# Optimization experiments

Hardware: AMD Instinct MI355X
Metric: run time of the kernel (lower is better)

Reference implementation:

```python
import jax, jax.numpy as jnp
import numpy as np

N_NODES = 100000
N_EDGES = 800000
N_GRAPHS = 4000
EMB = 128      # node_emb_dims
HID = 256      # hidden_dims
FP = 2048      # fingerprint_dims
FIELD_DIMS = {"atom_type": 120, "degree": 12, "charge": 10}


def setup_inputs() -> dict:
    key = jax.random.key(0)
    ks = iter(jax.random.split(key, 40))
    p = lambda shape: jax.random.normal(next(ks), shape, dtype=jnp.float32) * 0.02
    inp = {
        "atom_idx": jax.random.randint(next(ks), (N_NODES,), 0, FIELD_DIMS["atom_type"]),
        "degree_idx": jax.random.randint(next(ks), (N_NODES,), 0, FIELD_DIMS["degree"]),
        "charge_idx": jax.random.randint(next(ks), (N_NODES,), 0, FIELD_DIMS["charge"]),
        "edge_index": jax.random.randint(next(ks), (2, N_EDGES), 0, N_NODES),
        "batch": jnp.sort(jax.random.randint(next(ks), (N_NODES,), 0, N_GRAPHS)),
        "fingerprint": jax.random.normal(next(ks), (N_GRAPHS, FP), dtype=jnp.float32),
        # FFM projector params
        "emb_atom": p((FIELD_DIMS["atom_type"], EMB)),
        "emb_degree": p((FIELD_DIMS["degree"], EMB)),
        "emb_charge": p((FIELD_DIMS["charge"], EMB)),
        "proj_w1": p((3 * EMB, EMB)), "proj_b1": jnp.zeros((EMB,), jnp.float32),
        "proj_w2": p((EMB, EMB)), "proj_b2": jnp.zeros((EMB,), jnp.float32),
        # fingerprint linear
        "fp_w": p((FP, HID)), "fp_b": jnp.zeros((HID,), jnp.float32),
        # GCN layers
        "conv_w0": p((EMB, HID)), "conv_b0": jnp.zeros((HID,), jnp.float32),
        "conv_w1": p((HID, HID)), "conv_b1": jnp.zeros((HID,), jnp.float32),
        "conv_w2": p((HID, HID)), "conv_b2": jnp.zeros((HID,), jnp.float32),
        "conv_w3": p((HID, HID)), "conv_b3": jnp.zeros((HID,), jnp.float32),
        # head
        "lin1_w": p((2 * HID, HID // 2)), "lin1_b": jnp.zeros((HID // 2,), jnp.float32),
        "lin2_w": p((HID // 2, 1)), "lin2_b": jnp.zeros((1,), jnp.float32),
    }
    return inp


def gcn_conv(x, w, b, src, dst, n):
    # PyG GCNConv: linear, add self-loops, symmetric norm, scatter-add at dst, + bias
    xw = x @ w
    loop = jnp.arange(n)
    src_f = jnp.concatenate([src, loop])
    dst_f = jnp.concatenate([dst, loop])
    deg = jax.ops.segment_sum(jnp.ones_like(dst_f, dtype=x.dtype), dst_f, num_segments=n)
    dinv = jax.lax.rsqrt(deg)  # deg >= 1 thanks to self-loops
    norm = dinv[src_f] * dinv[dst_f]                       # [E+N]
    msg = xw[src_f] * norm[:, None]                        # [E+N, HID]
    return jax.ops.segment_sum(msg, dst_f, num_segments=n) + b


def reference(atom_idx, degree_idx, charge_idx, edge_index, batch, fingerprint,
              emb_atom, emb_degree, emb_charge,
              proj_w1, proj_b1, proj_w2, proj_b2, fp_w, fp_b,
              conv_w0, conv_b0, conv_w1, conv_b1, conv_w2, conv_b2, conv_w3, conv_b3,
              lin1_w, lin1_b, lin2_w, lin2_b):
    # FieldAwareFactorizationMachine projector (vectorized over all nodes)
    e = jnp.concatenate([emb_atom[atom_idx], emb_degree[degree_idx], emb_charge[charge_idx]], axis=-1)
    h = jax.nn.relu(e @ proj_w1 + proj_b1) @ proj_w2 + proj_b2   # [N, EMB]
    src, dst = edge_index[0], edge_index[1]
    for w, b in ((conv_w0, conv_b0), (conv_w1, conv_b1), (conv_w2, conv_b2), (conv_w3, conv_b3)):
        h = jax.nn.relu(gcn_conv(h, w, b, src, dst, N_NODES))
    pooled = jax.ops.segment_sum(h, batch, num_segments=N_GRAPHS)  # scatter sum pooling
    fp_emb = fingerprint @ fp_w + fp_b
    z = jnp.concatenate([fp_emb, pooled], axis=-1)                 # [B, 2*HID]
    z = jax.nn.relu(z @ lin1_w + lin1_b)
    return z @ lin2_w + lin2_b                                     # [B, 1]
```

## Files before the change

kernel.cpp:

```cpp
#include <hip/hip_runtime.h>
#include <stdint.h>

#define NN 100000
#define NE 800000
#define NG 4000
#define NBLK ((NN + 255) / 256)

typedef __attribute__((ext_vector_type(8))) short s16x8;
typedef __attribute__((ext_vector_type(4))) float f32x4;
typedef __attribute__((ext_vector_type(2))) float f32x2;

__device__ __forceinline__ float b2f(unsigned short u) {
    return __uint_as_float(((unsigned int)u) << 16);
}
__device__ __forceinline__ unsigned short f2b(float f) {
    unsigned int x = __float_as_uint(f);
    x = x + 0x7FFFu + ((x >> 16) & 1u);
    return (unsigned short)(x >> 16);
}
__device__ __forceinline__ s16x8 cvt8(const float* __restrict__ p) {
    float4 a = *(const float4*)p;
    float4 b = *(const float4*)(p + 4);
    s16x8 r = {(short)f2b(a.x), (short)f2b(a.y), (short)f2b(a.z), (short)f2b(a.w),
               (short)f2b(b.x), (short)f2b(b.y), (short)f2b(b.z), (short)f2b(b.w)};
    return r;
}

__device__ __forceinline__ void gload16(const void* g, void* l) {
    __builtin_amdgcn_global_load_lds((const __attribute__((address_space(1))) unsigned int*)g,
                                     (__attribute__((address_space(3))) unsigned int*)l, 16, 0, 0);
}

__device__ __forceinline__ void acc8(f32x2* acc, s16x8 r) {
    const unsigned int* u = (const unsigned int*)&r;
#pragma unroll
    for (int q = 0; q < 4; ++q) {
        unsigned int w = u[q];
        f32x2 x;
        x[0] = __uint_as_float(w << 16);
        x[1] = __uint_as_float(w & 0xFFFF0000u);
        asm("v_pk_add_f32 %0, %1, %0" : "+v"(acc[q]) : "v"(x));
    }
}

__global__ void k_count(const int* __restrict__ dst, int* __restrict__ cnt) {
    int e = blockIdx.x * 256 + threadIdx.x;
    if (e < NE) atomicAdd(&cnt[dst[e]], 1);
}

__global__ void k_dinv(const int* __restrict__ cnt, float* __restrict__ dinv) {
    int n = blockIdx.x * 256 + threadIdx.x;
    if (n < NN) dinv[n] = rsqrtf((float)(cnt[n] + 1));
}

__global__ __launch_bounds__(256) void k_bsum(const int* __restrict__ cnt, int* __restrict__ bsum) {
    __shared__ int s[256];
    int i = blockIdx.x * 256 + threadIdx.x;
    s[threadIdx.x] = (i < NN) ? cnt[i] : 0;
    __syncthreads();
    for (int off = 128; off; off >>= 1) {
        if (threadIdx.x < off) s[threadIdx.x] += s[threadIdx.x + off];
        __syncthreads();
    }
    if (threadIdx.x == 0) bsum[blockIdx.x] = s[0];
}

__global__ __launch_bounds__(512) void k_bscan(const int* __restrict__ bsum, int* __restrict__ bpre) {
    __shared__ int s[512];
    int t = threadIdx.x;
    int v = (t < NBLK) ? bsum[t] : 0;
    s[t] = v;
    __syncthreads();
    for (int off = 1; off < 512; off <<= 1) {
        int u = (t >= off) ? s[t - off] : 0;
        __syncthreads();
        s[t] += u;
        __syncthreads();
    }
    if (t < NBLK) bpre[t] = s[t] - v;
}

__global__ __launch_bounds__(256) void k_rowptr(const int* __restrict__ cnt, const int* __restrict__ bpre,
                                                int* __restrict__ row_ptr, int* __restrict__ cursor) {
    __shared__ int s[256];
    int t = threadIdx.x;
    int i = blockIdx.x * 256 + t;
    int v = (i < NN) ? cnt[i] : 0;
    s[t] = v;
    __syncthreads();
    for (int off = 1; off < 256; off <<= 1) {
        int u = (t >= off) ? s[t - off] : 0;
        __syncthreads();
        s[t] += u;
        __syncthreads();
    }
    if (i < NN) {
        int excl = bpre[blockIdx.x] + s[t] - v;
        row_ptr[i] = excl;
        cursor[i] = excl;
        if (i == NN - 1) row_ptr[NN] = NE;
    }
}

__global__ void k_fill(const int* __restrict__ src, const int* __restrict__ dst,
                       int* __restrict__ cursor, int* __restrict__ colA) {
    int e = blockIdx.x * 256 + threadIdx.x;
    if (e < NE) {
        int d = dst[e];
        int p = atomicAdd(&cursor[d], 1);
        colA[p] = src[e];
    }
}

__global__ void k_t(const float* __restrict__ src, unsigned short* __restrict__ dst, int KN, int ln) {
    int i = blockIdx.x * 256 + threadIdx.x;
    if (i < KN) {
        int k = i >> ln, n = i & ((1 << ln) - 1);
        dst[(size_t)n * (KN >> ln) + k] = f2b(src[i]);
    }
}

__global__ void k_cvt(const float* __restrict__ src, unsigned short* __restrict__ dst, int n8) {
    int i = blockIdx.x * 256 + threadIdx.x;
    if (i < n8) *(s16x8*)&dst[(size_t)i * 8] = cvt8(&src[(size_t)i * 8]);
}

__global__ void k_binit(float* __restrict__ fe, const float* __restrict__ b) {
    int i = blockIdx.x * 256 + threadIdx.x;
    fe[i] = b[i & 255];
}

__global__ void k_z(const float* __restrict__ fe, unsigned short* __restrict__ zcat) {
    int i = blockIdx.x * 256 + threadIdx.x;
    int g = i >> 8, c = i & 255;
    zcat[(size_t)g * 512 + c] = f2b(fe[i]);
}

template <bool GATHER, bool BIAS, bool RELU, bool CBF16>
__global__ __launch_bounds__(256) void k_mm(
    const unsigned short* __restrict__ A, const unsigned short* __restrict__ Bt,
    void* __restrict__ Cv, const float* __restrict__ bias, int M, int N, int K,
    const int* __restrict__ ai, const int* __restrict__ di, const int* __restrict__ ci,
    const float* __restrict__ ea, const float* __restrict__ ed, const float* __restrict__ ec) {
    __shared__ unsigned short As[128 * 40];
    __shared__ unsigned short Bs[128 * 40];
    const int tid = threadIdx.x;
    const int row0 = blockIdx.x * 128, col0 = blockIdx.y * 128;
    const int lane = tid & 63, wid = tid >> 6;
    const int wrow = (wid >> 1) * 64, wcol = (wid & 1) * 64;
    const int lr = lane & 15, lk8 = (lane >> 4) * 8;

    const int sr = tid >> 1;
    const int skc = (tid & 1) * 16;
    const int agrow = row0 + sr;
    const int bgrow = col0 + sr;
    int ia = 0, idg = 0, ic = 0;
    if (GATHER && agrow < M) { ia = ai[agrow] * 128; idg = di[agrow] * 128; ic = ci[agrow] * 128; }

    f32x4 acc[4][4] = {};

    for (int kb = 0; kb < K; kb += 32) {
        if (kb) __syncthreads();
#pragma unroll
        for (int c = 0; c < 2; ++c) {
            int kloc = skc + c * 8;
            s16x8 v = {};
            if (agrow < M) {
                if (GATHER) {
                    int kg = kb + kloc;
                    const float* p = (kg < 128) ? (ea + ia + kg)
                                   : (kg < 256) ? (ed + idg + kg - 128)
                                                : (ec + ic + kg - 256);
                    v = cvt8(p);
                } else {
                    v = *(const s16x8*)&A[(size_t)agrow * K + kb + kloc];
                }
            }
            *(s16x8*)&As[sr * 40 + kloc] = v;
            s16x8 w = *(const s16x8*)&Bt[(size_t)bgrow * K + kb + kloc];
            *(s16x8*)&Bs[sr * 40 + kloc] = w;
        }
        __syncthreads();
        s16x8 af[4], bfr[4];
#pragma unroll
        for (int f = 0; f < 4; ++f)
            af[f] = *(const s16x8*)&As[(wrow + f * 16 + lr) * 40 + lk8];
#pragma unroll
        for (int f = 0; f < 4; ++f)
            bfr[f] = *(const s16x8*)&Bs[(wcol + f * 16 + lr) * 40 + lk8];
#pragma unroll
        for (int fm = 0; fm < 4; ++fm)
#pragma unroll
            for (int fn = 0; fn < 4; ++fn)
                acc[fm][fn] = __builtin_amdgcn_mfma_f32_16x16x32_bf16(af[fm], bfr[fn], acc[fm][fn], 0, 0, 0);
    }
#pragma unroll
    for (int fm = 0; fm < 4; ++fm) {
#pragma unroll
        for (int r = 0; r < 4; ++r) {
            int row = row0 + wrow + fm * 16 + (lane >> 4) * 4 + r;
            if (row < M) {
#pragma unroll
                for (int fn = 0; fn < 4; ++fn) {
                    int col = col0 + wcol + fn * 16 + lr;
                    float v = acc[fm][fn][r];
                    if (BIAS) v += bias[col];
                    if (RELU) v = fmaxf(v, 0.f);
                    if (CBF16) ((unsigned short*)Cv)[(size_t)row * N + col] = f2b(v);
                    else       ((float*)Cv)[(size_t)row * N + col] = v;
                }
            }
        }
    }
}

template <bool BIAS, bool RELU, bool CBF16, bool SPLITK, bool PRES>
__global__ __launch_bounds__(256) void k_mmA(
    const unsigned short* __restrict__ A, const unsigned short* __restrict__ Bt,
    void* __restrict__ Cv, const float* __restrict__ bias, const float* __restrict__ pres,
    int M, int N, int K, int kc) {
    __shared__ unsigned short As[128 * 32];
    __shared__ unsigned short Bs[128 * 32];
    const int tid = threadIdx.x;
    const int row0 = blockIdx.x * 128, col0 = blockIdx.y * 128;
    const int lane = tid & 63, wid = tid >> 6;
    const int wrow = (wid >> 1) * 64, wcol = (wid & 1) * 64;
    const int lr = lane & 15, lk8 = (lane >> 4) * 8;

    const int k0 = SPLITK ? blockIdx.z * kc : 0;
    const int k1 = SPLITK ? k0 + kc : K;

    const int sra = wid * 32 + (lane >> 2);
    const int sca = (lane & 3) * 8;
    const unsigned short* a0 = A + (size_t)min(row0 + sra, M - 1) * K + sca;
    const unsigned short* a1 = A + (size_t)min(row0 + sra + 16, M - 1) * K + sca;
    const unsigned short* b0 = Bt + (size_t)(col0 + sra) * K + sca;
    const unsigned short* b1 = Bt + (size_t)(col0 + sra + 16) * K + sca;
    unsigned short* lA0 = &As[(wid * 2 + 0) * 512];
    unsigned short* lA1 = &As[(wid * 2 + 1) * 512];
    unsigned short* lB0 = &Bs[(wid * 2 + 0) * 512];
    unsigned short* lB1 = &Bs[(wid * 2 + 1) * 512];

    f32x4 acc[4][4] = {};

    for (int kb = k0; kb < k1; kb += 32) {
        if (kb != k0) __syncthreads();
        gload16(a0 + kb, lA0);
        gload16(a1 + kb, lA1);
        gload16(b0 + kb, lB0);
        gload16(b1 + kb, lB1);
        __syncthreads();
        s16x8 af[4], bfr[4];
#pragma unroll
        for (int f = 0; f < 4; ++f)
            af[f] = *(const s16x8*)&As[(wrow + f * 16 + lr) * 32 + lk8];
#pragma unroll
        for (int f = 0; f < 4; ++f)
            bfr[f] = *(const s16x8*)&Bs[(wcol + f * 16 + lr) * 32 + lk8];
#pragma unroll
        for (int fm = 0; fm < 4; ++fm)
#pragma unroll
            for (int fn = 0; fn < 4; ++fn)
                acc[fm][fn] = __builtin_amdgcn_mfma_f32_16x16x32_bf16(af[fm], bfr[fn], acc[fm][fn], 0, 0, 0);
    }
#pragma unroll
    for (int fm = 0; fm < 4; ++fm) {
#pragma unroll
        for (int r = 0; r < 4; ++r) {
            int row = row0 + wrow + fm * 16 + (lane >> 4) * 4 + r;
            if (row < M) {
                float pr = PRES ? pres[row] : 1.f;
#pragma unroll
                for (int fn = 0; fn < 4; ++fn) {
                    int col = col0 + wcol + fn * 16 + lr;
                    float v = acc[fm][fn][r];
                    if (SPLITK) {
                        atomicAdd(&((float*)Cv)[(size_t)row * N + col], v);
                    } else {
                        if (BIAS) v += bias[col];
                        if (RELU) v = fmaxf(v, 0.f);
                        if (PRES) v *= pr;
                        if (CBF16) ((unsigned short*)Cv)[(size_t)row * N + col] = f2b(v);
                        else       ((float*)Cv)[(size_t)row * N + col] = v;
                    }
                }
            }
        }
    }
}

template <int WPN, bool FUSE>
__global__ __launch_bounds__(256) void k_scat2(const unsigned short* __restrict__ xw,
                                               unsigned short* __restrict__ hout,
                                               const float* __restrict__ dinv,
                                               const int* __restrict__ row_ptr,
                                               const int* __restrict__ colA,
                                               const float* __restrict__ bias) {
    constexpr int W = WPN * 128;
    const int wid = threadIdx.x >> 6, lane = threadIdx.x & 63;
    const int gw = blockIdx.x * 4 + wid;
    const int v = (WPN == 2) ? (gw >> 1) : gw;
    const int cs = (WPN == 2) ? (gw & 1) * 128 : 0;
    const int grp = lane >> 4, li = lane & 15;
    const int c0 = cs + li * 8;

    f32x2 acc[4] = {};
    const int beg = row_ptr[v], end = row_ptr[v + 1];
    int p = beg + grp;
    for (; p + 4 < end; p += 8) {
        int s0 = colA[p], s1 = colA[p + 4];
        s16x8 r0 = *(const s16x8*)&xw[(size_t)s0 * W + c0];
        s16x8 r1 = *(const s16x8*)&xw[(size_t)s1 * W + c0];
        acc8(acc, r0);
        acc8(acc, r1);
    }
    if (p < end) {
        int s0 = colA[p];
        s16x8 r0 = *(const s16x8*)&xw[(size_t)s0 * W + c0];
        acc8(acc, r0);
    }

    const float dv = dinv[v];
    s16x8 rs = *(const s16x8*)&xw[(size_t)v * W + c0];
    unsigned short o[8];
#pragma unroll
    for (int q = 0; q < 4; ++q) {
#pragma unroll
        for (int h = 0; h < 2; ++h) {
            float a = acc[q][h];
            a += __shfl_xor(a, 16);
            a += __shfl_xor(a, 32);
            a += b2f((unsigned short)rs[2 * q + h]);
            a *= dv;
            if (FUSE) a = fmaxf(a + bias[c0 + 2 * q + h], 0.f);
            o[2 * q + h] = f2b(a);
        }
    }
    if (grp == 0) *(s16x8*)&hout[(size_t)v * W + c0] = *(const s16x8*)o;
}

__global__ void k_bounds(const int* __restrict__ batch, int* __restrict__ gstart) {
    int n = blockIdx.x * 256 + threadIdx.x;
    if (n >= NN) return;
    int b = batch[n];
    if (n == 0) {
        for (int g = 0; g <= b; ++g) gstart[g] = 0;
    } else {
        int pb = batch[n - 1];
        if (pb != b)
            for (int g = pb + 1; g <= b; ++g) gstart[g] = n;
    }
    if (n == NN - 1) {
        for (int g = b + 1; g <= NG; ++g) gstart[g] = NN;
    }
}

__global__ __launch_bounds__(64) void k_pool(const unsigned short* __restrict__ h,
                                             const int* __restrict__ gstart,
                                             unsigned short* __restrict__ zcat) {
    int g = blockIdx.x;
    int lane = threadIdx.x;
    int c0 = lane * 4;
    int beg = gstart[g], end = gstart[g + 1];
    float a0 = 0.f, a1 = 0.f, a2 = 0.f, a3 = 0.f;
    for (int n = beg; n < end; ++n) {
        ushort4 r = *(const ushort4*)&h[(size_t)n * 256 + c0];
        a0 += b2f(r.x); a1 += b2f(r.y); a2 += b2f(r.z); a3 += b2f(r.w);
    }
    ushort4 o;
    o.x = f2b(a0); o.y = f2b(a1); o.z = f2b(a2); o.w = f2b(a3);
    *(ushort4*)&zcat[(size_t)g * 512 + 256 + c0] = o;
}

__global__ __launch_bounds__(256) void k_dot(const float* __restrict__ z1,
                                             const float* __restrict__ w2,
                                             const float* __restrict__ b2,
                                             float* __restrict__ out) {
    int wid = threadIdx.x >> 6, lane = threadIdx.x & 63;
    int g = blockIdx.x * 4 + wid;
    float s = z1[(size_t)g * 128 + lane] * w2[lane]
            + z1[(size_t)g * 128 + 64 + lane] * w2[64 + lane];
#pragma unroll
    for (int off = 32; off; off >>= 1) s += __shfl_xor(s, off);
    if (lane == 0) out[g] = s + b2[0];
}

extern "C" void kernel_launch(void* const* d_in, const int* in_sizes, int n_in,
                              void* d_out, int out_size, void* d_ws, size_t ws_size,
                              hipStream_t stream) {
    const int* atom_idx   = (const int*)d_in[0];
    const int* degree_idx = (const int*)d_in[1];
    const int* charge_idx = (const int*)d_in[2];
    const int* edge_index = (const int*)d_in[3];
    const int* batch      = (const int*)d_in[4];
    const float* fingerprint = (const float*)d_in[5];
    const float* emb_atom   = (const float*)d_in[6];
    const float* emb_degree = (const float*)d_in[7];
    const float* emb_charge = (const float*)d_in[8];
    const float* proj_w1 = (const float*)d_in[9];
    const float* proj_b1 = (const float*)d_in[10];
    const float* proj_w2 = (const float*)d_in[11];
    const float* proj_b2 = (const float*)d_in[12];
    const float* fp_w = (const float*)d_in[13];
    const float* fp_b = (const float*)d_in[14];
    const float* conv_w[4] = {(const float*)d_in[15], (const float*)d_in[17],
                              (const float*)d_in[19], (const float*)d_in[21]};
    const float* conv_b[4] = {(const float*)d_in[16], (const float*)d_in[18],
                              (const float*)d_in[20], (const float*)d_in[22]};
    const float* lin1_w = (const float*)d_in[23];
    const float* lin1_b = (const float*)d_in[24];
    const float* lin2_w = (const float*)d_in[25];
    const float* lin2_b = (const float*)d_in[26];
    float* out = (float*)d_out;

    const int* src = edge_index;
    const int* dst = edge_index + NE;

    char* p = (char*)d_ws;
    auto carve = [&](size_t bytes) { void* r = (void*)p; p += (bytes + 255) & ~(size_t)255; return r; };
    unsigned short* bufA = (unsigned short*)carve((size_t)NN * 256 * 2);
    unsigned short* bufB = (unsigned short*)carve((size_t)NN * 256 * 2);
    int*   cnt     = (int*)carve((size_t)NN * 4);
    float* dinv    = (float*)carve((size_t)NN * 4);
    int*   row_ptr = (int*)carve((size_t)(NN + 1) * 4);
    int*   cursor  = (int*)carve((size_t)(NN + 1) * 4);
    int*   colA    = (int*)carve((size_t)NE * 4);
    int*   gstart  = (int*)carve((size_t)(NG + 1) * 4);
    float* fp_emb  = (float*)carve((size_t)NG * 256 * 4);
    int*   bsum    = (int*)carve((size_t)NBLK * 4);
    int*   bpre    = (int*)carve((size_t)NBLK * 4);
    unsigned short* w1t  = (unsigned short*)carve((size_t)128 * 384 * 2);
    unsigned short* w2t  = (unsigned short*)carve((size_t)128 * 128 * 2);
    unsigned short* cwt[4];
    cwt[0] = (unsigned short*)carve((size_t)256 * 128 * 2);
    for (int l = 1; l < 4; ++l) cwt[l] = (unsigned short*)carve((size_t)256 * 256 * 2);
    unsigned short* fpwt = (unsigned short*)carve((size_t)256 * 2048 * 2);
    unsigned short* fpbf = (unsigned short*)carve((size_t)NG * 2048 * 2);
    unsigned short* l1wt = (unsigned short*)carve((size_t)128 * 512 * 2);
    unsigned short* zcat = (unsigned short*)carve((size_t)NG * 512 * 2);
    float* z1      = (float*)carve((size_t)NG * 128 * 4);

    hipMemsetAsync(cnt, 0, (size_t)NN * 4, stream);
    k_count<<<(NE + 255) / 256, 256, 0, stream>>>(dst, cnt);
    k_dinv<<<(NN + 255) / 256, 256, 0, stream>>>(cnt, dinv);
    k_bsum<<<NBLK, 256, 0, stream>>>(cnt, bsum);
    k_bscan<<<1, 512, 0, stream>>>(bsum, bpre);
    k_rowptr<<<NBLK, 256, 0, stream>>>(cnt, bpre, row_ptr, cursor);
    k_fill<<<(NE + 255) / 256, 256, 0, stream>>>(src, dst, cursor, colA);

    k_t<<<(49152 + 255) / 256, 256, 0, stream>>>(proj_w1, w1t, 49152, 7);
    k_t<<<(16384 + 255) / 256, 256, 0, stream>>>(proj_w2, w2t, 16384, 7);
    k_t<<<(32768 + 255) / 256, 256, 0, stream>>>(conv_w[0], cwt[0], 32768, 8);
    for (int l = 1; l < 4; ++l)
        k_t<<<(65536 + 255) / 256, 256, 0, stream>>>(conv_w[l], cwt[l], 65536, 8);
    k_t<<<(524288 + 255) / 256, 256, 0, stream>>>(fp_w, fpwt, 524288, 8);
    k_t<<<(65536 + 255) / 256, 256, 0, stream>>>(lin1_w, l1wt, 65536, 7);
    k_cvt<<<(NG * 2048 / 8 + 255) / 256, 256, 0, stream>>>(fingerprint, fpbf, NG * 2048 / 8);

    k_binit<<<NG, 256, 0, stream>>>(fp_emb, fp_b);
    k_mmA<false, false, false, true, false><<<dim3((NG + 127) / 128, 2, 4), 256, 0, stream>>>(
        fpbf, fpwt, fp_emb, nullptr, nullptr, NG, 256, 2048, 512);
    k_z<<<NG, 256, 0, stream>>>(fp_emb, zcat);

    const int mg = (NN + 127) / 128;

    k_mm<true, true, true, true><<<dim3(mg, 1), 256, 0, stream>>>(
        nullptr, w1t, bufA, proj_b1, NN, 128, 384,
        atom_idx, degree_idx, charge_idx, emb_atom, emb_degree, emb_charge);
    k_mmA<true, false, true, false, true><<<dim3(mg, 1), 256, 0, stream>>>(
        bufA, w2t, bufB, proj_b2, dinv, NN, 128, 128, 0);

    k_scat2<1, false><<<NN / 4, 256, 0, stream>>>(bufB, bufA, dinv, row_ptr, colA, nullptr);
    k_mmA<true, true, true, false, false><<<dim3(mg, 2), 256, 0, stream>>>(
        bufA, cwt[0], bufB, conv_b[0], nullptr, NN, 256, 128, 0);

    for (int l = 1; l < 4; ++l) {
        k_mmA<false, false, true, false, true><<<dim3(mg, 2), 256, 0, stream>>>(
            bufB, cwt[l], bufA, nullptr, dinv, NN, 256, 256, 0);
        k_scat2<2, true><<<NN / 2, 256, 0, stream>>>(bufA, bufB, dinv, row_ptr, colA, conv_b[l]);
    }

    k_bounds<<<(NN + 255) / 256, 256, 0, stream>>>(batch, gstart);
    k_pool<<<NG, 64, 0, stream>>>(bufB, gstart, zcat);

    k_mmA<true, true, false, false, false><<<dim3((NG + 127) / 128, 1), 256, 0, stream>>>(
        zcat, l1wt, z1, lin1_b, nullptr, NG, 128, 512, 0);
    k_dot<<<NG / 4, 256, 0, stream>>>(z1, lin2_w, lin2_b, out);
}
```

Before: 789.8 us.

## Double-buffer GEMM LDS tiles and assign one node per 16-lane group in scatter

The GEMM kernel now keeps two LDS buffers, so it can start loading the next K tile while the MFMAs run on the current one, and it needs one barrier per iteration instead of two. The scatter kernel now maps each 16-lane group (or pair of groups for width 256) to its own destination node rather than a whole wave per node, which removes the cross-group shuffle reduction and the idle lanes when degrees are small. This raises per-wave parallelism across nodes at the cost of more divergence between groups with different degrees and double the LDS use in the GEMM.

After: 749.1 us. 1.05x faster.

```diff
diff --git a/kernel.cpp b/kernel.cpp
--- a/kernel.cpp
+++ b/kernel.cpp
@@ -219,8 +219,8 @@
     const unsigned short* __restrict__ A, const unsigned short* __restrict__ Bt,
     void* __restrict__ Cv, const float* __restrict__ bias, const float* __restrict__ pres,
     int M, int N, int K, int kc) {
-    __shared__ unsigned short As[128 * 32];
-    __shared__ unsigned short Bs[128 * 32];
+    __shared__ unsigned short As[2][128 * 32];
+    __shared__ unsigned short Bs[2][128 * 32];
     const int tid = threadIdx.x;
     const int row0 = blockIdx.x * 128, col0 = blockIdx.y * 128;
     const int lane = tid & 63, wid = tid >> 6;
@@ -228,40 +228,48 @@
     const int lr = lane & 15, lk8 = (lane >> 4) * 8;
 
     const int k0 = SPLITK ? blockIdx.z * kc : 0;
-    const int k1 = SPLITK ? k0 + kc : K;
+    const int nt = (SPLITK ? kc : K) / 32;
 
     const int sra = wid * 32 + (lane >> 2);
     const int sca = (lane & 3) * 8;
-    const unsigned short* a0 = A + (size_t)min(row0 + sra, M - 1) * K + sca;
-    const unsigned short* a1 = A + (size_t)min(row0 + sra + 16, M - 1) * K + sca;
-    const unsigned short* b0 = Bt + (size_t)(col0 + sra) * K + sca;
-    const unsigned short* b1 = Bt + (size_t)(col0 + sra + 16) * K + sca;
-    unsigned short* lA0 = &As[(wid * 2 + 0) * 512];
-    unsigned short* lA1 = &As[(wid * 2 + 1) * 512];
-    unsigned short* lB0 = &Bs[(wid * 2 + 0) * 512];
-    unsigned short* lB1 = &Bs[(wid * 2 + 1) * 512];
+    const unsigned short* a0 = A + (size_t)min(row0 + sra, M - 1) * K + sca + k0;
+    const unsigned short* a1 = A + (size_t)min(row0 + sra + 16, M - 1) * K + sca + k0;
+    const unsigned short* b0 = Bt + (size_t)(col0 + sra) * K + sca + k0;
+    const unsigned short* b1 = Bt + (size_t)(col0 + sra + 16) * K + sca + k0;
+    const int lo0 = (wid * 2 + 0) * 512;
+    const int lo1 = (wid * 2 + 1) * 512;
 
     f32x4 acc[4][4] = {};
 
-    for (int kb = k0; kb < k1; kb += 32) {
-        if (kb != k0) __syncthreads();
-        gload16(a0 + kb, lA0);
-        gload16(a1 + kb, lA1);
-        gload16(b0 + kb, lB0);
-        gload16(b1 + kb, lB1);
-        __syncthreads();
+    gload16(a0, &As[0][lo0]);
+    gload16(a1, &As[0][lo1]);
+    gload16(b0, &Bs[0][lo0]);
+    gload16(b1, &Bs[0][lo1]);
+    __syncthreads();
+
+    int cur = 0;
+    for (int t = 0; t < nt; ++t) {
+        if (t + 1 < nt) {
+            int kb = (t + 1) * 32;
+            gload16(a0 + kb, &As[cur ^ 1][lo0]);
+            gload16(a1 + kb, &As[cur ^ 1][lo1]);
+            gload16(b0 + kb, &Bs[cur ^ 1][lo0]);
+            gload16(b1 + kb, &Bs[cur ^ 1][lo1]);
+        }
         s16x8 af[4], bfr[4];
 #pragma unroll
         for (int f = 0; f < 4; ++f)
-            af[f] = *(const s16x8*)&As[(wrow + f * 16 + lr) * 32 + lk8];
+            af[f] = *(const s16x8*)&As[cur][(wrow + f * 16 + lr) * 32 + lk8];
 #pragma unroll
         for (int f = 0; f < 4; ++f)
-            bfr[f] = *(const s16x8*)&Bs[(wcol + f * 16 + lr) * 32 + lk8];
+            bfr[f] = *(const s16x8*)&Bs[cur][(wcol + f * 16 + lr) * 32 + lk8];
 #pragma unroll
         for (int fm = 0; fm < 4; ++fm)
 #pragma unroll
             for (int fn = 0; fn < 4; ++fn)
                 acc[fm][fn] = __builtin_amdgcn_mfma_f32_16x16x32_bf16(af[fm], bfr[fn], acc[fm][fn], 0, 0, 0);
+        __syncthreads();
+        cur ^= 1;
     }
 #pragma unroll
     for (int fm = 0; fm < 4; ++fm) {
@@ -290,33 +298,32 @@
 }
 
 template <int WPN, bool FUSE>
-__global__ __launch_bounds__(256) void k_scat2(const unsigned short* __restrict__ xw,
+__global__ __launch_bounds__(256) void k_scat3(const unsigned short* __restrict__ xw,
                                                unsigned short* __restrict__ hout,
                                                const float* __restrict__ dinv,
                                                const int* __restrict__ row_ptr,
                                                const int* __restrict__ colA,
                                                const float* __restrict__ bias) {
     constexpr int W = WPN * 128;
+    constexpr int NPW = 4 / WPN;
     const int wid = threadIdx.x >> 6, lane = threadIdx.x & 63;
-    const int gw = blockIdx.x * 4 + wid;
-    const int v = (WPN == 2) ? (gw >> 1) : gw;
-    const int cs = (WPN == 2) ? (gw & 1) * 128 : 0;
     const int grp = lane >> 4, li = lane & 15;
+    const int v = (blockIdx.x * 4 + wid) * NPW + grp / WPN;
+    const int cs = (WPN == 2) ? (grp & 1) * 128 : 0;
     const int c0 = cs + li * 8;
 
     f32x2 acc[4] = {};
     const int beg = row_ptr[v], end = row_ptr[v + 1];
-    int p = beg + grp;
-    for (; p + 4 < end; p += 8) {
-        int s0 = colA[p], s1 = colA[p + 4];
+    int p = beg;
+    for (; p + 1 < end; p += 2) {
+        int s0 = colA[p], s1 = colA[p + 1];
         s16x8 r0 = *(const s16x8*)&xw[(size_t)s0 * W + c0];
         s16x8 r1 = *(const s16x8*)&xw[(size_t)s1 * W + c0];
         acc8(acc, r0);
         acc8(acc, r1);
     }
     if (p < end) {
-        int s0 = colA[p];
-        s16x8 r0 = *(const s16x8*)&xw[(size_t)s0 * W + c0];
+        s16x8 r0 = *(const s16x8*)&xw[(size_t)colA[p] * W + c0];
         acc8(acc, r0);
     }
 
@@ -324,19 +331,14 @@
     s16x8 rs = *(const s16x8*)&xw[(size_t)v * W + c0];
     unsigned short o[8];
 #pragma unroll
-    for (int q = 0; q < 4; ++q) {
-#pragma unroll
-        for (int h = 0; h < 2; ++h) {
-            float a = acc[q][h];
-            a += __shfl_xor(a, 16);
-            a += __shfl_xor(a, 32);
-            a += b2f((unsigned short)rs[2 * q + h]);
-            a *= dv;
-            if (FUSE) a = fmaxf(a + bias[c0 + 2 * q + h], 0.f);
-            o[2 * q + h] = f2b(a);
-        }
-    }
-    if (grp == 0) *(s16x8*)&hout[(size_t)v * W + c0] = *(const s16x8*)o;
+    for (int j = 0; j < 8; ++j) {
+        float a = acc[j >> 1][j & 1];
+        a += b2f((unsigned short)rs[j]);
+        a *= dv;
+        if (FUSE) a = fmaxf(a + bias[c0 + j], 0.f);
+        o[j] = f2b(a);
+    }
+    *(s16x8*)&hout[(size_t)v * W + c0] = *(const s16x8*)o;
 }
 
 __global__ void k_bounds(const int* __restrict__ batch, int* __restrict__ gstart) {
@@ -470,14 +472,14 @@
     k_mmA<true, false, true, false, true><<<dim3(mg, 1), 256, 0, stream>>>(
         bufA, w2t, bufB, proj_b2, dinv, NN, 128, 128, 0);
 
-    k_scat2<1, false><<<NN / 4, 256, 0, stream>>>(bufB, bufA, dinv, row_ptr, colA, nullptr);
+    k_scat3<1, false><<<NN / 16, 256, 0, stream>>>(bufB, bufA, dinv, row_ptr, colA, nullptr);
     k_mmA<true, true, true, false, false><<<dim3(mg, 2), 256, 0, stream>>>(
         bufA, cwt[0], bufB, conv_b[0], nullptr, NN, 256, 128, 0);
 
     for (int l = 1; l < 4; ++l) {
         k_mmA<false, false, true, false, true><<<dim3(mg, 2), 256, 0, stream>>>(
             bufB, cwt[l], bufA, nullptr, dinv, NN, 256, 256, 0);
-        k_scat2<2, true><<<NN / 2, 256, 0, stream>>>(bufA, bufB, dinv, row_ptr, colA, conv_b[l]);
+        k_scat3<2, true><<<NN / 8, 256, 0, stream>>>(bufA, bufB, dinv, row_ptr, colA, conv_b[l]);
     }
 
     k_bounds<<<(NN + 255) / 256, 256, 0, stream>>>(batch, gstart);
```
